# Optimization experiments

Measured on AMD Instinct MI355X. Metric: run time of the kernel, lower is better.

## Reference

```python
import jax, jax.numpy as jnp
import numpy as np

B, T, M = 4, 1024, 512
H, K, V = 8, 64, 64
EPS = 1e-6


def setup_inputs() -> dict:
    key = jax.random.key(0)
    ks = jax.random.split(key, 8)
    s = 1.0 / np.sqrt(M)
    return {
        "query": jax.random.normal(ks[0], (B, T, M), jnp.float32),
        "key": jax.random.normal(ks[1], (B, T, M), jnp.float32),
        "value": jax.random.normal(ks[2], (B, T, M), jnp.float32),
        "Wq": jax.random.normal(ks[3], (M, H * K), jnp.float32) * s,
        "Wk": jax.random.normal(ks[4], (M, H * K), jnp.float32) * s,
        "Wv": jax.random.normal(ks[5], (M, H * V), jnp.float32) * s,
        # gate linear is zero-initialized in the original (Constant(0.0)); use
        # small random weights so the gate path is exercised numerically.
        "Wg": jax.random.normal(ks[6], (M, H * V), jnp.float32) * (0.02 * s),
        "bg": jnp.zeros((H * V,), jnp.float32),
        "Wo": jax.random.normal(ks[7], (H * V, M), jnp.float32) * (1.0 / np.sqrt(H * V)),
    }


def _phi(x):
    return jax.nn.elu(x) + 1.0


def reference(query, key, value, Wq, Wk, Wv, Wg, bg, Wo):
    # projections -> [B, T, H, d]
    q = (query @ Wq).reshape(B, T, H, K)
    k = (key @ Wk).reshape(B, T, H, K)
    v = (value @ Wv).reshape(B, T, H, V)

    qf = _phi(q)
    kf = _phi(k)

    # multiplicative value gate from the raw value input
    gate = jax.nn.sigmoid((value @ Wg + bg).reshape(B, T, H, V))
    v = v * (2.0 * gate)

    # visualization attention map: qf . kf, causal, row-normalized
    scores = jnp.einsum("bthk,bshk->bhts", qf, kf)  # [B,H,T,T]
    causal = (jnp.arange(T)[None, :] <= jnp.arange(T)[:, None]).astype(scores.dtype)
    scores = scores * causal[None, None]
    att_map = scores / (jnp.sum(scores, axis=-1, keepdims=True) + EPS)

    # causal linear attention via cumulative sums (Tq == Tk so the idx-take
    # in the original is an identity gather)
    kv = jnp.einsum("bthk,bthv->bthkv", kf, v)  # [B,T,H,K,V]
    kv_cum = jnp.cumsum(kv, axis=1)
    k_cum = jnp.cumsum(kf, axis=1)               # [B,T,H,K]

    numer = jnp.einsum("bthk,bthkv->bthv", qf, kv_cum)
    denom = jnp.einsum("bthk,bthk->bth", qf, k_cum) + EPS
    out = (numer / denom[..., None]).reshape(B, T, H * V)
    out = out @ Wo  # [B,T,M]
    return out, att_map
```

## Files before the change

### kernel.cpp

```cpp
#include <hip/hip_runtime.h>
#include <cstdint>

#define TDIM 1024
#define BDIM 4
#define EPSF 1e-6f

#define OFF_DEN   0u
#define OFF_KSUM  32768u
#define OFF_KV    65536u
#define FLOAT_BYTES 8650752u
#define UOFF_QP 0u
#define UOFF_KP 2097152u
#define UOFF_VP 4194304u
#define UOFF_NB 6291456u
#define UOFF_WQ 8388608u
#define UOFF_WK 8650752u
#define UOFF_WV 8912896u
#define UOFF_WG 9175040u
#define UOFF_WO 9437184u

typedef short bf16x8 __attribute__((ext_vector_type(8)));
typedef float f32x4  __attribute__((ext_vector_type(4)));
typedef unsigned short ushort_t;

union bfu { int4 i4; unsigned short us[8]; bf16x8 v; };

__device__ __forceinline__ float phi_f(float x)  { return x > 0.f ? x + 1.f : __expf(x); }
__device__ __forceinline__ float sigm_f(float x) { return 1.f / (1.f + __expf(-x)); }
__device__ __forceinline__ unsigned short f2b(float x) {
    union { float f; unsigned u; } v; v.f = x;
    return (unsigned short)((v.u + 0x7FFFu + ((v.u >> 16) & 1u)) >> 16);
}
__device__ __forceinline__ float b2f(unsigned short s) {
    union { unsigned u; float f; } v; v.u = (unsigned)s << 16; return v.f;
}
__device__ __forceinline__ int4 pack8(float4 a, float4 b) {
    bfu u;
    u.us[0] = f2b(a.x); u.us[1] = f2b(a.y); u.us[2] = f2b(a.z); u.us[3] = f2b(a.w);
    u.us[4] = f2b(b.x); u.us[5] = f2b(b.y); u.us[6] = f2b(b.z); u.us[7] = f2b(b.w);
    return u.i4;
}
#define FMA4(ACC, S, V) do { (ACC).x += (S)*(V).x; (ACC).y += (S)*(V).y; \
                             (ACC).z += (S)*(V).z; (ACC).w += (S)*(V).w; } while (0)

__global__ __launch_bounds__(256) void castwt_all(const float* __restrict__ W0,
                                                  const float* __restrict__ W1,
                                                  const float* __restrict__ W2,
                                                  const float* __restrict__ W3,
                                                  const float* __restrict__ W4,
                                                  ushort_t* __restrict__ T0,
                                                  ushort_t* __restrict__ T1,
                                                  ushort_t* __restrict__ T2,
                                                  ushort_t* __restrict__ T3,
                                                  ushort_t* __restrict__ T4) {
    const float* W; ushort_t* Wt;
    switch (blockIdx.z) {
        case 0: W = W0; Wt = T0; break;
        case 1: W = W1; Wt = T1; break;
        case 2: W = W2; Wt = T2; break;
        case 3: W = W3; Wt = T3; break;
        default: W = W4; Wt = T4; break;
    }
    __shared__ unsigned short tile[32][36];
    const int t = threadIdx.x;
    const int r0 = blockIdx.y * 32, c0 = blockIdx.x * 32;
    {
        const int r = t >> 3, c4 = (t & 7) * 4;
        float4 x = *(const float4*)(W + (size_t)(r0 + r) * 512 + c0 + c4);
        tile[c4 + 0][r] = f2b(x.x); tile[c4 + 1][r] = f2b(x.y);
        tile[c4 + 2][r] = f2b(x.z); tile[c4 + 3][r] = f2b(x.w);
    }
    __syncthreads();
    const int c = t >> 3, r4 = (t & 7) * 4;
    ushort4 o;
    o.x = tile[c][r4 + 0]; o.y = tile[c][r4 + 1];
    o.z = tile[c][r4 + 2]; o.w = tile[c][r4 + 3];
    *(ushort4*)(Wt + (size_t)(c0 + c) * 512 + r0 + r4) = o;
}

__global__ __launch_bounds__(256) void proj_k(const float* __restrict__ query,
                                              const float* __restrict__ key_,
                                              const float* __restrict__ value,
                                              const ushort_t* __restrict__ wqt,
                                              const ushort_t* __restrict__ wkt,
                                              const ushort_t* __restrict__ wvt,
                                              const ushort_t* __restrict__ wgt,
                                              const float* __restrict__ bg,
                                              ushort_t* __restrict__ qp,
                                              ushort_t* __restrict__ kp,
                                              ushort_t* __restrict__ vp) {
    __shared__ __align__(16) unsigned short As[2][4096];
    __shared__ __align__(16) unsigned short Bs[2][4096];
    __shared__ __align__(16) unsigned short Bs2[2][4096];
    const int z = blockIdx.z;
    const float* A = (z == 0) ? query : (z == 1) ? key_ : value;
    const ushort_t* B0 = (z == 0) ? wqt : (z == 1) ? wkt : wvt;
    ushort_t* outp = (z == 0) ? qp : (z == 1) ? kp : vp;
    const bool dual = (z == 2);

    const int tid = threadIdx.x;
    const int row0 = blockIdx.x * 64, n0 = blockIdx.y * 64;
    const int w = tid >> 6, lane = tid & 63;
    const int cc = tid & 7, rr = tid >> 3;
    const int fm = lane & 15, fq = lane >> 4;
    const int la0 = (cc * 64 + (rr ^ cc)) * 8;
    const int la1 = (cc * 64 + ((rr + 32) ^ cc)) * 8;

    f32x4 acc[4], acc2[4];
#pragma unroll
    for (int i = 0; i < 4; i++) {
        acc[i]  = (f32x4){0.f, 0.f, 0.f, 0.f};
        acc2[i] = (f32x4){0.f, 0.f, 0.f, 0.f};
    }

    const float*   aptr = A  + (size_t)(row0 + rr) * 512 + cc * 8;
    const ushort_t* bptr = B0 + (size_t)(n0 + rr) * 512 + cc * 8;
    const ushort_t* gptr = wgt + (size_t)(n0 + rr) * 512 + cc * 8;

    float4 a0 = *(const float4*)(aptr);
    float4 a1 = *(const float4*)(aptr + 4);
    float4 a2 = *(const float4*)(aptr + 32 * 512);
    float4 a3 = *(const float4*)(aptr + 32 * 512 + 4);
    int4 b0 = *(const int4*)(bptr);
    int4 b1 = *(const int4*)(bptr + 32 * 512);
    int4 g0 = {0, 0, 0, 0}, g1 = {0, 0, 0, 0};
    if (dual) { g0 = *(const int4*)(gptr); g1 = *(const int4*)(gptr + 32 * 512); }
    *(int4*)&As[0][la0] = pack8(a0, a1);
    *(int4*)&As[0][la1] = pack8(a2, a3);
    *(int4*)&Bs[0][la0] = b0; *(int4*)&Bs[0][la1] = b1;
    if (dual) { *(int4*)&Bs2[0][la0] = g0; *(int4*)&Bs2[0][la1] = g1; }
    __syncthreads();

    for (int kti = 0; kti < 8; kti++) {
        const int buf = kti & 1;
        if (kti < 7) {
            const int off = (kti + 1) * 64;
            a0 = *(const float4*)(aptr + off);
            a1 = *(const float4*)(aptr + off + 4);
            a2 = *(const float4*)(aptr + off + 32 * 512);
            a3 = *(const float4*)(aptr + off + 32 * 512 + 4);
            b0 = *(const int4*)(bptr + off);
            b1 = *(const int4*)(bptr + off + 32 * 512);
            if (dual) {
                g0 = *(const int4*)(gptr + off);
                g1 = *(const int4*)(gptr + off + 32 * 512);
            }
        }
        if (dual) {
#pragma unroll
            for (int j = 0; j < 2; j++) {
                const int cu = j * 4 + fq;
                bf16x8 af = *(const bf16x8*)&As[buf][(cu * 64 + ((w * 16 + fm) ^ cu)) * 8];
#pragma unroll
                for (int nb = 0; nb < 4; nb++) {
                    bf16x8 bv = *(const bf16x8*)&Bs[buf][(cu * 64 + ((nb * 16 + fm) ^ cu)) * 8];
                    bf16x8 gv = *(const bf16x8*)&Bs2[buf][(cu * 64 + ((nb * 16 + fm) ^ cu)) * 8];
                    acc[nb]  = __builtin_amdgcn_mfma_f32_16x16x32_bf16(af, bv, acc[nb], 0, 0, 0);
                    acc2[nb] = __builtin_amdgcn_mfma_f32_16x16x32_bf16(af, gv, acc2[nb], 0, 0, 0);
                }
            }
        } else {
#pragma unroll
            for (int j = 0; j < 2; j++) {
                const int cu = j * 4 + fq;
                bf16x8 af = *(const bf16x8*)&As[buf][(cu * 64 + ((w * 16 + fm) ^ cu)) * 8];
#pragma unroll
                for (int nb = 0; nb < 4; nb++) {
                    bf16x8 bv = *(const bf16x8*)&Bs[buf][(cu * 64 + ((nb * 16 + fm) ^ cu)) * 8];
                    acc[nb] = __builtin_amdgcn_mfma_f32_16x16x32_bf16(af, bv, acc[nb], 0, 0, 0);
                }
            }
        }
        if (kti < 7) {
            const int nb_ = buf ^ 1;
            *(int4*)&As[nb_][la0] = pack8(a0, a1);
            *(int4*)&As[nb_][la1] = pack8(a2, a3);
            *(int4*)&Bs[nb_][la0] = b0; *(int4*)&Bs[nb_][la1] = b1;
            if (dual) { *(int4*)&Bs2[nb_][la0] = g0; *(int4*)&Bs2[nb_][la1] = g1; }
            __syncthreads();
        }
    }

#pragma unroll
    for (int nb = 0; nb < 4; nb++) {
        const int col = n0 + nb * 16 + fm;
        const float bb = dual ? bg[col] : 0.f;
#pragma unroll
        for (int r = 0; r < 4; r++) {
            const int row = row0 + w * 16 + fq * 4 + r;
            const float v = acc[nb][r];
            const ushort_t o = dual ? f2b(v * 2.f * sigm_f(acc2[nb][r] + bb))
                                    : f2b(phi_f(v));
            outp[(size_t)row * 512 + col] = o;
        }
    }
}

__global__ __launch_bounds__(256) void outproj_k(const ushort_t* __restrict__ A,
                                                 const ushort_t* __restrict__ Bt,
                                                 float* __restrict__ out) {
    __shared__ __align__(16) unsigned short As[2][4096];
    __shared__ __align__(16) unsigned short Bs[2][4096];
    const int tid = threadIdx.x;
    const int row0 = blockIdx.x * 64, n0 = blockIdx.y * 64;
    const int w = tid >> 6, lane = tid & 63;
    const int cc = tid & 7, rr = tid >> 3;
    const int fm = lane & 15, fq = lane >> 4;
    const int la0 = (cc * 64 + (rr ^ cc)) * 8;
    const int la1 = (cc * 64 + ((rr + 32) ^ cc)) * 8;

    f32x4 acc[4];
#pragma unroll
    for (int i = 0; i < 4; i++) acc[i] = (f32x4){0.f, 0.f, 0.f, 0.f};

    const ushort_t* aptr = A  + (size_t)(row0 + rr) * 512 + cc * 8;
    const ushort_t* bptr = Bt + (size_t)(n0 + rr) * 512 + cc * 8;
    int4 ra0 = *(const int4*)(aptr);
    int4 ra1 = *(const int4*)(aptr + 32 * 512);
    int4 rb0 = *(const int4*)(bptr);
    int4 rb1 = *(const int4*)(bptr + 32 * 512);
    *(int4*)&As[0][la0] = ra0; *(int4*)&As[0][la1] = ra1;
    *(int4*)&Bs[0][la0] = rb0; *(int4*)&Bs[0][la1] = rb1;
    __syncthreads();

    for (int kti = 0; kti < 8; kti++) {
        const int buf = kti & 1;
        if (kti < 7) {
            const int off = (kti + 1) * 64;
            ra0 = *(const int4*)(aptr + off);
            ra1 = *(const int4*)(aptr + off + 32 * 512);
            rb0 = *(const int4*)(bptr + off);
            rb1 = *(const int4*)(bptr + off + 32 * 512);
        }
#pragma unroll
        for (int j = 0; j < 2; j++) {
            const int cu = j * 4 + fq;
            bf16x8 af = *(const bf16x8*)&As[buf][(cu * 64 + ((w * 16 + fm) ^ cu)) * 8];
#pragma unroll
            for (int nb = 0; nb < 4; nb++) {
                bf16x8 bv = *(const bf16x8*)&Bs[buf][(cu * 64 + ((nb * 16 + fm) ^ cu)) * 8];
                acc[nb] = __builtin_amdgcn_mfma_f32_16x16x32_bf16(af, bv, acc[nb], 0, 0, 0);
            }
        }
        if (kti < 7) {
            const int nb_ = buf ^ 1;
            *(int4*)&As[nb_][la0] = ra0; *(int4*)&As[nb_][la1] = ra1;
            *(int4*)&Bs[nb_][la0] = rb0; *(int4*)&Bs[nb_][la1] = rb1;
            __syncthreads();
        }
    }
#pragma unroll
    for (int nb = 0; nb < 4; nb++) {
        const int col = n0 + nb * 16 + fm;
#pragma unroll
        for (int r = 0; r < 4; r++) {
            const int row = row0 + w * 16 + fq * 4 + r;
            __builtin_nontemporal_store(acc[nb][r], &out[(size_t)row * 512 + col]);
        }
    }
}

__global__ __launch_bounds__(256) void chunksum_k(const ushort_t* __restrict__ kb,
                                                  const ushort_t* __restrict__ vb,
                                                  float* __restrict__ kv,
                                                  float* __restrict__ ksum) {
    __shared__ __align__(16) float kf_c[64][68];
    __shared__ __align__(16) float vg_c[64][68];
    const int tid = threadIdx.x;
    const int bh = blockIdx.x, c = blockIdx.y;
    const int b = bh >> 3, h = bh & 7;
    const int r = tid >> 2, qq = tid & 3;
    {
        const size_t rowbase = ((size_t)(b * TDIM + c * 64 + r)) * 512 + h * 64 + qq * 16;
        bfu k0, k1, v0, v1;
        k0.i4 = *(const int4*)(kb + rowbase);
        k1.i4 = *(const int4*)(kb + rowbase + 8);
        v0.i4 = *(const int4*)(vb + rowbase);
        v1.i4 = *(const int4*)(vb + rowbase + 8);
#pragma unroll
        for (int j = 0; j < 8; j++) {
            kf_c[r][qq * 16 + j]     = b2f(k0.us[j]);
            kf_c[r][qq * 16 + 8 + j] = b2f(k1.us[j]);
            vg_c[r][qq * 16 + j]     = b2f(v0.us[j]);
            vg_c[r][qq * 16 + 8 + j] = b2f(v1.us[j]);
        }
    }
    __syncthreads();
    const int k0i = (tid >> 4) * 4;
    const int v0i = (tid & 15) * 4;
    float4 a4[4];
#pragma unroll
    for (int i = 0; i < 4; i++) a4[i] = make_float4(0.f, 0.f, 0.f, 0.f);
    for (int t = 0; t < 64; t++) {
        float4 kk4 = *(const float4*)&kf_c[t][k0i];
        float4 vv  = *(const float4*)&vg_c[t][v0i];
        FMA4(a4[0], kk4.x, vv); FMA4(a4[1], kk4.y, vv);
        FMA4(a4[2], kk4.z, vv); FMA4(a4[3], kk4.w, vv);
    }
    const size_t base = (size_t)(bh * 16 + c) * 64;
#pragma unroll
    for (int i = 0; i < 4; i++)
        *(float4*)(kv + (base + k0i + i) * 64 + v0i) = a4[i];
    if (tid < 64) {
        float s = 0.f;
        for (int t = 0; t < 64; t++) s += kf_c[t][tid];
        ksum[base + tid] = s;
    }
}

__global__ __launch_bounds__(256) void prefix_k(float* __restrict__ kv,
                                                float* __restrict__ ksum) {
    const int tid = threadIdx.x;
    const int bh = blockIdx.x;
    float4 run[4];
#pragma unroll
    for (int u = 0; u < 4; u++) run[u] = make_float4(0.f, 0.f, 0.f, 0.f);
    const int d0 = tid * 16;
    for (int c = 0; c < 16; c++) {
        float* p = kv + (size_t)(bh * 16 + c) * 4096 + d0;
#pragma unroll
        for (int u = 0; u < 4; u++) {
            float4 x = *(float4*)(p + 4 * u);
            *(float4*)(p + 4 * u) = run[u];
            run[u].x += x.x; run[u].y += x.y; run[u].z += x.z; run[u].w += x.w;
        }
    }
    if (tid < 64) {
        float r2 = 0.f;
        for (int c = 0; c < 16; c++) {
            float* p = ksum + (size_t)(bh * 16 + c) * 64 + tid;
            float x = *p; *p = r2; r2 += x;
        }
    }
}

__global__ __launch_bounds__(256) void chunkout_k(const ushort_t* __restrict__ qb,
                                                  const ushort_t* __restrict__ kb,
                                                  const ushort_t* __restrict__ vb,
                                                  const float* __restrict__ kvp,
                                                  const float* __restrict__ ksum,
                                                  ushort_t* __restrict__ nbo,
                                                  float* __restrict__ denom) {
    __shared__ __align__(16) unsigned short qs[4096];
    __shared__ __align__(16) unsigned short ks[4096];
    __shared__ __align__(16) unsigned short vs[4096];
    __shared__ __align__(16) unsigned short kvs[4096];
    __shared__ __align__(16) float sc[64][68];
    __shared__ __align__(16) float kpre[64];
    __shared__ __align__(16) float ps[64][4];
    __shared__ __align__(16) float inv_s[64];
    const int tid = threadIdx.x;
    const int bh = blockIdx.x, c = blockIdx.y;
    const int b = bh >> 3, h = bh & 7;
    const int w = tid >> 6, lane = tid & 63;
    const int fm = lane & 15, fq = lane >> 4;

    {
        const int rr = tid >> 3, cc = tid & 7;
        const ushort_t* qp = qb + ((size_t)(b * TDIM + c * 64 + rr)) * 512 + h * 64 + cc * 8;
        const ushort_t* kp = kb + ((size_t)(b * TDIM + c * 64 + rr)) * 512 + h * 64 + cc * 8;
        *(int4*)&qs[(cc * 64 + (rr ^ cc)) * 8]        = *(const int4*)qp;
        *(int4*)&qs[(cc * 64 + ((rr + 32) ^ cc)) * 8] = *(const int4*)(qp + 32 * 512);
        *(int4*)&ks[(cc * 64 + (rr ^ cc)) * 8]        = *(const int4*)kp;
        *(int4*)&ks[(cc * 64 + ((rr + 32) ^ cc)) * 8] = *(const int4*)(kp + 32 * 512);
        const int v = tid & 63, su0 = (tid >> 6) * 2;
#pragma unroll
        for (int e = 0; e < 2; e++) {
            const int su = su0 + e;
            bfu t1;
#pragma unroll
            for (int j = 0; j < 8; j++)
                t1.us[j] = vb[((size_t)(b * TDIM + c * 64 + su * 8 + j)) * 512 + h * 64 + v];
            *(int4*)&vs[(su * 64 + (v ^ su)) * 8] = t1.i4;
            bfu t2;
            const float* kvrow = kvp + (size_t)(bh * 16 + c) * 4096 + v;
#pragma unroll
            for (int j = 0; j < 8; j++)
                t2.us[j] = f2b(kvrow[(su * 8 + j) * 64]);
            *(int4*)&kvs[(su * 64 + (v ^ su)) * 8] = t2.i4;
        }
        if (tid < 64) kpre[tid] = ksum[(size_t)(bh * 16 + c) * 64 + tid];
    }
    __syncthreads();

    {
        f32x4 sa[4];
#pragma unroll
        for (int i = 0; i < 4; i++) sa[i] = (f32x4){0.f, 0.f, 0.f, 0.f};
#pragma unroll
        for (int j = 0; j < 2; j++) {
            const int cu = j * 4 + fq;
            bf16x8 aq = *(const bf16x8*)&qs[(cu * 64 + ((w * 16 + fm) ^ cu)) * 8];
#pragma unroll
            for (int nb = 0; nb < 4; nb++) {
                bf16x8 bk = *(const bf16x8*)&ks[(cu * 64 + ((nb * 16 + fm) ^ cu)) * 8];
                sa[nb] = __builtin_amdgcn_mfma_f32_16x16x32_bf16(aq, bk, sa[nb], 0, 0, 0);
            }
        }
#pragma unroll
        for (int nb = 0; nb < 4; nb++) {
            const int s_l = nb * 16 + fm;
#pragma unroll
            for (int r = 0; r < 4; r++) {
                const int t_l = w * 16 + fq * 4 + r;
                sc[t_l][s_l] = (s_l <= t_l) ? sa[nb][r] : 0.f;
            }
        }
    }
    __syncthreads();

    {
        const int rw = tid >> 2, sq = tid & 3;
        float p = 0.f;
#pragma unroll
        for (int s = sq * 16; s < sq * 16 + 16; s++) p += sc[rw][s];
#pragma unroll
        for (int kd = sq * 16; kd < sq * 16 + 16; kd++) {
            const int cu = kd >> 3;
            p += b2f(qs[(cu * 64 + (rw ^ cu)) * 8 + (kd & 7)]) * kpre[kd];
        }
        ps[rw][sq] = p;
    }
    __syncthreads();
    {
        const int rw = tid >> 2, sq = tid & 3;
        if (sq == 0) {
            float den = ps[rw][0] + ps[rw][1] + ps[rw][2] + ps[rw][3];
            denom[(size_t)bh * TDIM + c * 64 + rw] = den;
            inv_s[rw] = 1.f / (den + EPSF);
        }
    }
    __syncthreads();

    {
        f32x4 oa[4];
#pragma unroll
        for (int i = 0; i < 4; i++) oa[i] = (f32x4){0.f, 0.f, 0.f, 0.f};
        bf16x8 aq[2], ap_[2];
#pragma unroll
        for (int j = 0; j < 2; j++) {
            const int cu = j * 4 + fq;
            aq[j] = *(const bf16x8*)&qs[(cu * 64 + ((w * 16 + fm) ^ cu)) * 8];
            bfu t;
#pragma unroll
            for (int e2 = 0; e2 < 8; e2++) t.us[e2] = f2b(sc[w * 16 + fm][cu * 8 + e2]);
            ap_[j] = t.v;
        }
#pragma unroll
        for (int nb = 0; nb < 4; nb++) {
#pragma unroll
            for (int j = 0; j < 2; j++) {
                const int cu = j * 4 + fq;
                bf16x8 bkv = *(const bf16x8*)&kvs[(cu * 64 + ((nb * 16 + fm) ^ cu)) * 8];
                bf16x8 bv  = *(const bf16x8*)&vs[(cu * 64 + ((nb * 16 + fm) ^ cu)) * 8];
                oa[nb] = __builtin_amdgcn_mfma_f32_16x16x32_bf16(aq[j], bkv, oa[nb], 0, 0, 0);
                oa[nb] = __builtin_amdgcn_mfma_f32_16x16x32_bf16(ap_[j], bv, oa[nb], 0, 0, 0);
            }
        }
#pragma unroll
        for (int nb = 0; nb < 4; nb++) {
            const int vcol = nb * 16 + fm;
#pragma unroll
            for (int r = 0; r < 4; r++) {
                const int t_l = w * 16 + fq * 4 + r;
                const float val = oa[nb][r] * inv_s[t_l];
                nbo[((size_t)(b * TDIM + c * 64 + t_l)) * 512 + h * 64 + vcol] = f2b(val);
            }
        }
    }
}

__global__ __launch_bounds__(256) void attmap_k(const ushort_t* __restrict__ qb,
                                                const ushort_t* __restrict__ kb,
                                                const float* __restrict__ denom,
                                                float* __restrict__ att) {
    __shared__ __align__(16) unsigned short qs[4096];
    __shared__ __align__(16) unsigned short ks[2][4096];
    __shared__ __align__(16) float inv_s[64];
    const int tid = threadIdx.x;
    const int bh = blockIdx.x, diag = blockIdx.y;
    const int tt0 = diag * 64;
    const int b = bh >> 3, h = bh & 7;
    const int w = tid >> 6, lane = tid & 63;
    const int fm = lane & 15, fq = lane >> 4;
    const int rr = tid >> 3, cc = tid & 7;
    const int la0 = (cc * 64 + (rr ^ cc)) * 8;
    const int la1 = (cc * 64 + ((rr + 32) ^ cc)) * 8;

    const ushort_t* qptr = qb + ((size_t)(b * TDIM + tt0 + rr)) * 512 + h * 64 + cc * 8;
    const ushort_t* kbase = kb + ((size_t)(b * TDIM + rr)) * 512 + h * 64 + cc * 8;
    *(int4*)&qs[la0] = *(const int4*)qptr;
    *(int4*)&qs[la1] = *(const int4*)(qptr + 32 * 512);
    int4 rk0 = *(const int4*)(kbase);
    int4 rk1 = *(const int4*)(kbase + 32 * 512);
    *(int4*)&ks[0][la0] = rk0;
    *(int4*)&ks[0][la1] = rk1;
    if (tid < 64) inv_s[tid] = 1.f / (denom[(size_t)bh * TDIM + tt0 + tid] + EPSF);
    __syncthreads();

    bf16x8 aq[2];
    float invr[4];
#pragma unroll
    for (int j = 0; j < 2; j++) {
        const int cu = j * 4 + fq;
        aq[j] = *(const bf16x8*)&qs[(cu * 64 + ((w * 16 + fm) ^ cu)) * 8];
    }
#pragma unroll
    for (int r = 0; r < 4; r++) invr[r] = inv_s[w * 16 + fq * 4 + r];

    float* attb = att + (size_t)bh * TDIM * TDIM;
    for (int st = 0; st <= diag; st++) {
        const int buf = st & 1;
        if (st < diag) {
            const size_t off = (size_t)(st + 1) * 64 * 512;
            rk0 = *(const int4*)(kbase + off);
            rk1 = *(const int4*)(kbase + off + 32 * 512);
        }
        f32x4 sa[4];
#pragma unroll
        for (int i = 0; i < 4; i++) sa[i] = (f32x4){0.f, 0.f, 0.f, 0.f};
#pragma unroll
        for (int j = 0; j < 2; j++) {
            const int cu = j * 4 + fq;
#pragma unroll
            for (int nb = 0; nb < 4; nb++) {
                bf16x8 bk = *(const bf16x8*)&ks[buf][(cu * 64 + ((nb * 16 + fm) ^ cu)) * 8];
                sa[nb] = __builtin_amdgcn_mfma_f32_16x16x32_bf16(aq[j], bk, sa[nb], 0, 0, 0);
            }
        }
        const int s0 = st * 64;
        if (st < diag) {
#pragma unroll
            for (int nb = 0; nb < 4; nb++) {
                const int s_g = s0 + nb * 16 + fm;
#pragma unroll
                for (int r = 0; r < 4; r++) {
                    const int t_g = tt0 + w * 16 + fq * 4 + r;
                    __builtin_nontemporal_store(sa[nb][r] * invr[r],
                                                &attb[(size_t)t_g * TDIM + s_g]);
                }
            }
            *(int4*)&ks[buf ^ 1][la0] = rk0;
            *(int4*)&ks[buf ^ 1][la1] = rk1;
            __syncthreads();
        } else {
#pragma unroll
            for (int nb = 0; nb < 4; nb++) {
                const int s_l = nb * 16 + fm;
#pragma unroll
                for (int r = 0; r < 4; r++) {
                    const int t_l = w * 16 + fq * 4 + r;
                    const float val = (s_l <= t_l) ? sa[nb][r] * invr[r] : 0.f;
                    __builtin_nontemporal_store(val,
                        &attb[(size_t)(tt0 + t_l) * TDIM + s0 + s_l]);
                }
            }
        }
    }
    {
        const f32x4 z = (f32x4){0.f, 0.f, 0.f, 0.f};
        const int r = tid >> 2, qq = tid & 3;
        float* rowp = attb + (size_t)(tt0 + r) * TDIM;
        for (int c0 = (diag + 1) * 64 + qq * 4; c0 < TDIM; c0 += 16)
            __builtin_nontemporal_store(z, (f32x4*)(rowp + c0));
    }
}

extern "C" void kernel_launch(void* const* d_in, const int* in_sizes, int n_in,
                              void* d_out, int out_size, void* d_ws, size_t ws_size,
                              hipStream_t stream) {
    (void)in_sizes; (void)n_in; (void)out_size; (void)ws_size;
    const float* query = (const float*)d_in[0];
    const float* key   = (const float*)d_in[1];
    const float* value = (const float*)d_in[2];
    const float* Wq    = (const float*)d_in[3];
    const float* Wk    = (const float*)d_in[4];
    const float* Wv    = (const float*)d_in[5];
    const float* Wg    = (const float*)d_in[6];
    const float* bg    = (const float*)d_in[7];
    const float* Wo    = (const float*)d_in[8];
    float* out = (float*)d_out;
    float* att = (float*)d_out + 2097152;
    float* ws  = (float*)d_ws;
    float* den  = ws + OFF_DEN;
    float* ksum = ws + OFF_KSUM;
    float* kv   = ws + OFF_KV;
    ushort_t* ub  = (ushort_t*)((char*)d_ws + FLOAT_BYTES);
    ushort_t* qp  = ub + UOFF_QP;
    ushort_t* kp  = ub + UOFF_KP;
    ushort_t* vp  = ub + UOFF_VP;
    ushort_t* nbp = ub + UOFF_NB;
    ushort_t* wqt = ub + UOFF_WQ;
    ushort_t* wkt = ub + UOFF_WK;
    ushort_t* wvt = ub + UOFF_WV;
    ushort_t* wgt = ub + UOFF_WG;
    ushort_t* wot = ub + UOFF_WO;

    dim3 blk(256);
    castwt_all<<<dim3(16, 16, 5), blk, 0, stream>>>(Wq, Wk, Wv, Wg, Wo,
                                                    wqt, wkt, wvt, wgt, wot);
    proj_k<<<dim3(64, 8, 3), blk, 0, stream>>>(query, key, value,
                                               wqt, wkt, wvt, wgt, bg, qp, kp, vp);
    chunksum_k<<<dim3(32, 16), blk, 0, stream>>>(kp, vp, kv, ksum);
    prefix_k<<<dim3(32), blk, 0, stream>>>(kv, ksum);
    chunkout_k<<<dim3(32, 16), blk, 0, stream>>>(qp, kp, vp, kv, ksum, nbp, den);
    attmap_k<<<dim3(32, 16), blk, 0, stream>>>(qp, kp, den, att);
    outproj_k<<<dim3(64, 8), blk, 0, stream>>>(nbp, wot, out);
}
```

Before: 266.1 us.

## Fuse prefix scan, chunk output and attention-map kernels into one kernel

Replaces the prefix_k, chunkout_k and attmap_k kernels with a single fused_k kernel. Each block recomputes its exclusive prefix of chunk KV states and k-sums by summing the earlier chunks directly, which removes the serial prefix kernel. It also reuses the diagonal score tile for the denominator, the output and the attention-map row, and schedules the heaviest diagonals first. In exchange it does redundant prefix summation of up to 15 chunk states per block and uses about 70 KB of dynamic shared memory, which may limit occupancy.

Measured after the change: 245.0 us. 7.9% less time.

```diff
diff --git a/kernel.cpp b/kernel.cpp
--- a/kernel.cpp
+++ b/kernel.cpp
@@ -5,7 +5,6 @@
 #define BDIM 4
 #define EPSF 1e-6f
 
-#define OFF_DEN   0u
 #define OFF_KSUM  32768u
 #define OFF_KV    65536u
 #define FLOAT_BYTES 8650752u
@@ -308,177 +307,25 @@
     }
 }
 
-__global__ __launch_bounds__(256) void prefix_k(float* __restrict__ kv,
-                                                float* __restrict__ ksum) {
+__global__ __launch_bounds__(256) void fused_k(const ushort_t* __restrict__ qb,
+                                               const ushort_t* __restrict__ kb,
+                                               const ushort_t* __restrict__ vb,
+                                               const float* __restrict__ kvc,
+                                               const float* __restrict__ ksum,
+                                               ushort_t* __restrict__ nbo,
+                                               float* __restrict__ att) {
+    extern __shared__ __align__(16) char smem[];
+    unsigned short* qs   = (unsigned short*)smem;
+    unsigned short* ksb  = qs + 4096;
+    unsigned short* vrow = ksb + 8192;
+    float* kvf  = (float*)(vrow + 64 * 72);
+    float* sc   = kvf + 64 * 68;
+    float* kpre = sc + 64 * 68;
+    float* ps   = kpre + 64;
+    float* inv_s = ps + 256;
+
     const int tid = threadIdx.x;
-    const int bh = blockIdx.x;
-    float4 run[4];
-#pragma unroll
-    for (int u = 0; u < 4; u++) run[u] = make_float4(0.f, 0.f, 0.f, 0.f);
-    const int d0 = tid * 16;
-    for (int c = 0; c < 16; c++) {
-        float* p = kv + (size_t)(bh * 16 + c) * 4096 + d0;
-#pragma unroll
-        for (int u = 0; u < 4; u++) {
-            float4 x = *(float4*)(p + 4 * u);
-            *(float4*)(p + 4 * u) = run[u];
-            run[u].x += x.x; run[u].y += x.y; run[u].z += x.z; run[u].w += x.w;
-        }
-    }
-    if (tid < 64) {
-        float r2 = 0.f;
-        for (int c = 0; c < 16; c++) {
-            float* p = ksum + (size_t)(bh * 16 + c) * 64 + tid;
-            float x = *p; *p = r2; r2 += x;
-        }
-    }
-}
-
-__global__ __launch_bounds__(256) void chunkout_k(const ushort_t* __restrict__ qb,
-                                                  const ushort_t* __restrict__ kb,
-                                                  const ushort_t* __restrict__ vb,
-                                                  const float* __restrict__ kvp,
-                                                  const float* __restrict__ ksum,
-                                                  ushort_t* __restrict__ nbo,
-                                                  float* __restrict__ denom) {
-    __shared__ __align__(16) unsigned short qs[4096];
-    __shared__ __align__(16) unsigned short ks[4096];
-    __shared__ __align__(16) unsigned short vs[4096];
-    __shared__ __align__(16) unsigned short kvs[4096];
-    __shared__ __align__(16) float sc[64][68];
-    __shared__ __align__(16) float kpre[64];
-    __shared__ __align__(16) float ps[64][4];
-    __shared__ __align__(16) float inv_s[64];
-    const int tid = threadIdx.x;
-    const int bh = blockIdx.x, c = blockIdx.y;
-    const int b = bh >> 3, h = bh & 7;
-    const int w = tid >> 6, lane = tid & 63;
-    const int fm = lane & 15, fq = lane >> 4;
-
-    {
-        const int rr = tid >> 3, cc = tid & 7;
-        const ushort_t* qp = qb + ((size_t)(b * TDIM + c * 64 + rr)) * 512 + h * 64 + cc * 8;
-        const ushort_t* kp = kb + ((size_t)(b * TDIM + c * 64 + rr)) * 512 + h * 64 + cc * 8;
-        *(int4*)&qs[(cc * 64 + (rr ^ cc)) * 8]        = *(const int4*)qp;
-        *(int4*)&qs[(cc * 64 + ((rr + 32) ^ cc)) * 8] = *(const int4*)(qp + 32 * 512);
-        *(int4*)&ks[(cc * 64 + (rr ^ cc)) * 8]        = *(const int4*)kp;
-        *(int4*)&ks[(cc * 64 + ((rr + 32) ^ cc)) * 8] = *(const int4*)(kp + 32 * 512);
-        const int v = tid & 63, su0 = (tid >> 6) * 2;
-#pragma unroll
-        for (int e = 0; e < 2; e++) {
-            const int su = su0 + e;
-            bfu t1;
-#pragma unroll
-            for (int j = 0; j < 8; j++)
-                t1.us[j] = vb[((size_t)(b * TDIM + c * 64 + su * 8 + j)) * 512 + h * 64 + v];
-            *(int4*)&vs[(su * 64 + (v ^ su)) * 8] = t1.i4;
-            bfu t2;
-            const float* kvrow = kvp + (size_t)(bh * 16 + c) * 4096 + v;
-#pragma unroll
-            for (int j = 0; j < 8; j++)
-                t2.us[j] = f2b(kvrow[(su * 8 + j) * 64]);
-            *(int4*)&kvs[(su * 64 + (v ^ su)) * 8] = t2.i4;
-        }
-        if (tid < 64) kpre[tid] = ksum[(size_t)(bh * 16 + c) * 64 + tid];
-    }
-    __syncthreads();
-
-    {
-        f32x4 sa[4];
-#pragma unroll
-        for (int i = 0; i < 4; i++) sa[i] = (f32x4){0.f, 0.f, 0.f, 0.f};
-#pragma unroll
-        for (int j = 0; j < 2; j++) {
-            const int cu = j * 4 + fq;
-            bf16x8 aq = *(const bf16x8*)&qs[(cu * 64 + ((w * 16 + fm) ^ cu)) * 8];
-#pragma unroll
-            for (int nb = 0; nb < 4; nb++) {
-                bf16x8 bk = *(const bf16x8*)&ks[(cu * 64 + ((nb * 16 + fm) ^ cu)) * 8];
-                sa[nb] = __builtin_amdgcn_mfma_f32_16x16x32_bf16(aq, bk, sa[nb], 0, 0, 0);
-            }
-        }
-#pragma unroll
-        for (int nb = 0; nb < 4; nb++) {
-            const int s_l = nb * 16 + fm;
-#pragma unroll
-            for (int r = 0; r < 4; r++) {
-                const int t_l = w * 16 + fq * 4 + r;
-                sc[t_l][s_l] = (s_l <= t_l) ? sa[nb][r] : 0.f;
-            }
-        }
-    }
-    __syncthreads();
-
-    {
-        const int rw = tid >> 2, sq = tid & 3;
-        float p = 0.f;
-#pragma unroll
-        for (int s = sq * 16; s < sq * 16 + 16; s++) p += sc[rw][s];
-#pragma unroll
-        for (int kd = sq * 16; kd < sq * 16 + 16; kd++) {
-            const int cu = kd >> 3;
-            p += b2f(qs[(cu * 64 + (rw ^ cu)) * 8 + (kd & 7)]) * kpre[kd];
-        }
-        ps[rw][sq] = p;
-    }
-    __syncthreads();
-    {
-        const int rw = tid >> 2, sq = tid & 3;
-        if (sq == 0) {
-            float den = ps[rw][0] + ps[rw][1] + ps[rw][2] + ps[rw][3];
-            denom[(size_t)bh * TDIM + c * 64 + rw] = den;
-            inv_s[rw] = 1.f / (den + EPSF);
-        }
-    }
-    __syncthreads();
-
-    {
-        f32x4 oa[4];
-#pragma unroll
-        for (int i = 0; i < 4; i++) oa[i] = (f32x4){0.f, 0.f, 0.f, 0.f};
-        bf16x8 aq[2], ap_[2];
-#pragma unroll
-        for (int j = 0; j < 2; j++) {
-            const int cu = j * 4 + fq;
-            aq[j] = *(const bf16x8*)&qs[(cu * 64 + ((w * 16 + fm) ^ cu)) * 8];
-            bfu t;
-#pragma unroll
-            for (int e2 = 0; e2 < 8; e2++) t.us[e2] = f2b(sc[w * 16 + fm][cu * 8 + e2]);
-            ap_[j] = t.v;
-        }
-#pragma unroll
-        for (int nb = 0; nb < 4; nb++) {
-#pragma unroll
-            for (int j = 0; j < 2; j++) {
-                const int cu = j * 4 + fq;
-                bf16x8 bkv = *(const bf16x8*)&kvs[(cu * 64 + ((nb * 16 + fm) ^ cu)) * 8];
-                bf16x8 bv  = *(const bf16x8*)&vs[(cu * 64 + ((nb * 16 + fm) ^ cu)) * 8];
-                oa[nb] = __builtin_amdgcn_mfma_f32_16x16x32_bf16(aq[j], bkv, oa[nb], 0, 0, 0);
-                oa[nb] = __builtin_amdgcn_mfma_f32_16x16x32_bf16(ap_[j], bv, oa[nb], 0, 0, 0);
-            }
-        }
-#pragma unroll
-        for (int nb = 0; nb < 4; nb++) {
-            const int vcol = nb * 16 + fm;
-#pragma unroll
-            for (int r = 0; r < 4; r++) {
-                const int t_l = w * 16 + fq * 4 + r;
-                const float val = oa[nb][r] * inv_s[t_l];
-                nbo[((size_t)(b * TDIM + c * 64 + t_l)) * 512 + h * 64 + vcol] = f2b(val);
-            }
-        }
-    }
-}
-
-__global__ __launch_bounds__(256) void attmap_k(const ushort_t* __restrict__ qb,
-                                                const ushort_t* __restrict__ kb,
-                                                const float* __restrict__ denom,
-                                                float* __restrict__ att) {
-    __shared__ __align__(16) unsigned short qs[4096];
-    __shared__ __align__(16) unsigned short ks[2][4096];
-    __shared__ __align__(16) float inv_s[64];
-    const int tid = threadIdx.x;
-    const int bh = blockIdx.x, diag = blockIdx.y;
+    const int bh = blockIdx.x, diag = 15 - (int)blockIdx.y;
     const int tt0 = diag * 64;
     const int b = bh >> 3, h = bh & 7;
     const int w = tid >> 6, lane = tid & 63;
@@ -487,16 +334,139 @@
     const int la0 = (cc * 64 + (rr ^ cc)) * 8;
     const int la1 = (cc * 64 + ((rr + 32) ^ cc)) * 8;
 
-    const ushort_t* qptr = qb + ((size_t)(b * TDIM + tt0 + rr)) * 512 + h * 64 + cc * 8;
     const ushort_t* kbase = kb + ((size_t)(b * TDIM + rr)) * 512 + h * 64 + cc * 8;
-    *(int4*)&qs[la0] = *(const int4*)qptr;
-    *(int4*)&qs[la1] = *(const int4*)(qptr + 32 * 512);
-    int4 rk0 = *(const int4*)(kbase);
-    int4 rk1 = *(const int4*)(kbase + 32 * 512);
-    *(int4*)&ks[0][la0] = rk0;
-    *(int4*)&ks[0][la1] = rk1;
-    if (tid < 64) inv_s[tid] = 1.f / (denom[(size_t)bh * TDIM + tt0 + tid] + EPSF);
-    __syncthreads();
+
+    {
+        const ushort_t* qptr = qb + ((size_t)(b * TDIM + tt0 + rr)) * 512 + h * 64 + cc * 8;
+        *(int4*)&qs[la0] = *(const int4*)qptr;
+        *(int4*)&qs[la1] = *(const int4*)(qptr + 32 * 512);
+        const ushort_t* kptr = kbase + (size_t)tt0 * 512;
+        *(int4*)&ksb[la0] = *(const int4*)kptr;
+        *(int4*)&ksb[la1] = *(const int4*)(kptr + 32 * 512);
+        const int r = tid >> 2, qq = tid & 3;
+        const ushort_t* vptr = vb + ((size_t)(b * TDIM + tt0 + r)) * 512 + h * 64 + qq * 16;
+        *(int4*)&vrow[r * 72 + qq * 16]     = *(const int4*)vptr;
+        *(int4*)&vrow[r * 72 + qq * 16 + 8] = *(const int4*)(vptr + 8);
+        float4 a4[4];
+#pragma unroll
+        for (int u = 0; u < 4; u++) a4[u] = make_float4(0.f, 0.f, 0.f, 0.f);
+        for (int c2 = 0; c2 < diag; c2++) {
+            const float* p = kvc + (size_t)(bh * 16 + c2) * 4096 + r * 64 + qq * 16;
+#pragma unroll
+            for (int u = 0; u < 4; u++) {
+                float4 x = *(const float4*)(p + 4 * u);
+                a4[u].x += x.x; a4[u].y += x.y; a4[u].z += x.z; a4[u].w += x.w;
+            }
+        }
+#pragma unroll
+        for (int u = 0; u < 4; u++) *(float4*)&kvf[r * 68 + qq * 16 + 4 * u] = a4[u];
+        if (tid < 64) {
+            float s = 0.f;
+            for (int c2 = 0; c2 < diag; c2++)
+                s += ksum[(size_t)(bh * 16 + c2) * 64 + tid];
+            kpre[tid] = s;
+        }
+    }
+    __syncthreads();
+
+    f32x4 sa[4];
+    {
+        int4 rk0 = {0,0,0,0}, rk1 = {0,0,0,0};
+        if (diag > 0) {
+            rk0 = *(const int4*)(kbase);
+            rk1 = *(const int4*)(kbase + 32 * 512);
+        }
+#pragma unroll
+        for (int i = 0; i < 4; i++) sa[i] = (f32x4){0.f, 0.f, 0.f, 0.f};
+#pragma unroll
+        for (int j = 0; j < 2; j++) {
+            const int cu = j * 4 + fq;
+            bf16x8 aqf = *(const bf16x8*)&qs[(cu * 64 + ((w * 16 + fm) ^ cu)) * 8];
+#pragma unroll
+            for (int nb = 0; nb < 4; nb++) {
+                bf16x8 bk = *(const bf16x8*)&ksb[(cu * 64 + ((nb * 16 + fm) ^ cu)) * 8];
+                sa[nb] = __builtin_amdgcn_mfma_f32_16x16x32_bf16(aqf, bk, sa[nb], 0, 0, 0);
+            }
+        }
+#pragma unroll
+        for (int nb = 0; nb < 4; nb++) {
+            const int s_l = nb * 16 + fm;
+#pragma unroll
+            for (int r = 0; r < 4; r++) {
+                const int t_l = w * 16 + fq * 4 + r;
+                sc[t_l * 68 + s_l] = (s_l <= t_l) ? sa[nb][r] : 0.f;
+            }
+        }
+        if (diag > 0) {
+            *(int4*)&ksb[4096 + la0] = rk0;
+            *(int4*)&ksb[4096 + la1] = rk1;
+        }
+    }
+    __syncthreads();
+
+    {
+        const int rw = tid >> 2, sq = tid & 3;
+        float p = 0.f;
+#pragma unroll
+        for (int s = sq * 16; s < sq * 16 + 16; s++) p += sc[rw * 68 + s];
+#pragma unroll
+        for (int kd = sq * 16; kd < sq * 16 + 16; kd++) {
+            const int cu = kd >> 3;
+            p += b2f(qs[(cu * 64 + (rw ^ cu)) * 8 + (kd & 7)]) * kpre[kd];
+        }
+        ps[rw * 4 + sq] = p;
+    }
+    __syncthreads();
+    {
+        const int rw = tid >> 2, sq = tid & 3;
+        if (sq == 0) {
+            float den = ps[rw * 4] + ps[rw * 4 + 1] + ps[rw * 4 + 2] + ps[rw * 4 + 3];
+            inv_s[rw] = 1.f / (den + EPSF);
+        }
+    }
+    __syncthreads();
+
+    {
+        f32x4 oa[4];
+#pragma unroll
+        for (int i = 0; i < 4; i++) oa[i] = (f32x4){0.f, 0.f, 0.f, 0.f};
+        bf16x8 aqv[2], apv[2];
+#pragma unroll
+        for (int j = 0; j < 2; j++) {
+            const int cu = j * 4 + fq;
+            aqv[j] = *(const bf16x8*)&qs[(cu * 64 + ((w * 16 + fm) ^ cu)) * 8];
+            bfu t;
+#pragma unroll
+            for (int e2 = 0; e2 < 8; e2++) t.us[e2] = f2b(sc[(w * 16 + fm) * 68 + cu * 8 + e2]);
+            apv[j] = t.v;
+        }
+#pragma unroll
+        for (int nb = 0; nb < 4; nb++) {
+            const int v = nb * 16 + fm;
+#pragma unroll
+            for (int j = 0; j < 2; j++) {
+                const int cu = j * 4 + fq;
+                bfu tkv, tv;
+#pragma unroll
+                for (int e = 0; e < 8; e++) {
+                    tkv.us[e] = f2b(kvf[(cu * 8 + e) * 68 + v]);
+                    tv.us[e]  = vrow[(cu * 8 + e) * 72 + v];
+                }
+                oa[nb] = __builtin_amdgcn_mfma_f32_16x16x32_bf16(aqv[j], tkv.v, oa[nb], 0, 0, 0);
+                oa[nb] = __builtin_amdgcn_mfma_f32_16x16x32_bf16(apv[j], tv.v, oa[nb], 0, 0, 0);
+            }
+        }
+#pragma unroll
+        for (int nb = 0; nb < 4; nb++) {
+            const int vcol = nb * 16 + fm;
+#pragma unroll
+            for (int r = 0; r < 4; r++) {
+                const int t_l = w * 16 + fq * 4 + r;
+                const float val = oa[nb][r] * inv_s[t_l];
+                nbo[((size_t)(b * TDIM + tt0 + t_l)) * 512 + h * 64 + vcol] = f2b(val);
+            }
+        }
+    }
 
     bf16x8 aq[2];
     float invr[4];
@@ -509,52 +479,53 @@
     for (int r = 0; r < 4; r++) invr[r] = inv_s[w * 16 + fq * 4 + r];
 
     float* attb = att + (size_t)bh * TDIM * TDIM;
-    for (int st = 0; st <= diag; st++) {
-        const int buf = st & 1;
-        if (st < diag) {
+    int4 rk0, rk1;
+    for (int st = 0; st < diag; st++) {
+        const int bsel = (st + 1) & 1;
+        if (st + 1 < diag) {
             const size_t off = (size_t)(st + 1) * 64 * 512;
             rk0 = *(const int4*)(kbase + off);
             rk1 = *(const int4*)(kbase + off + 32 * 512);
         }
-        f32x4 sa[4];
-#pragma unroll
-        for (int i = 0; i < 4; i++) sa[i] = (f32x4){0.f, 0.f, 0.f, 0.f};
+        f32x4 pa[4];
+#pragma unroll
+        for (int i = 0; i < 4; i++) pa[i] = (f32x4){0.f, 0.f, 0.f, 0.f};
 #pragma unroll
         for (int j = 0; j < 2; j++) {
             const int cu = j * 4 + fq;
 #pragma unroll
             for (int nb = 0; nb < 4; nb++) {
-                bf16x8 bk = *(const bf16x8*)&ks[buf][(cu * 64 + ((nb * 16 + fm) ^ cu)) * 8];
-                sa[nb] = __builtin_amdgcn_mfma_f32_16x16x32_bf16(aq[j], bk, sa[nb], 0, 0, 0);
+                bf16x8 bk = *(const bf16x8*)&ksb[bsel * 4096 +
+                                                 (cu * 64 + ((nb * 16 + fm) ^ cu)) * 8];
+                pa[nb] = __builtin_amdgcn_mfma_f32_16x16x32_bf16(aq[j], bk, pa[nb], 0, 0, 0);
             }
         }
         const int s0 = st * 64;
-        if (st < diag) {
-#pragma unroll
-            for (int nb = 0; nb < 4; nb++) {
-                const int s_g = s0 + nb * 16 + fm;
-#pragma unroll
-                for (int r = 0; r < 4; r++) {
-                    const int t_g = tt0 + w * 16 + fq * 4 + r;
-                    __builtin_nontemporal_store(sa[nb][r] * invr[r],
-                                                &attb[(size_t)t_g * TDIM + s_g]);
-                }
-            }
-            *(int4*)&ks[buf ^ 1][la0] = rk0;
-            *(int4*)&ks[buf ^ 1][la1] = rk1;
+#pragma unroll
+        for (int nb = 0; nb < 4; nb++) {
+            const int s_g = s0 + nb * 16 + fm;
+#pragma unroll
+            for (int r = 0; r < 4; r++) {
+                const int t_g = tt0 + w * 16 + fq * 4 + r;
+                __builtin_nontemporal_store(pa[nb][r] * invr[r],
+                                            &attb[(size_t)t_g * TDIM + s_g]);
+            }
+        }
+        if (st + 1 < diag) {
+            *(int4*)&ksb[(bsel ^ 1) * 4096 + la0] = rk0;
+            *(int4*)&ksb[(bsel ^ 1) * 4096 + la1] = rk1;
             __syncthreads();
-        } else {
-#pragma unroll
-            for (int nb = 0; nb < 4; nb++) {
-                const int s_l = nb * 16 + fm;
-#pragma unroll
-                for (int r = 0; r < 4; r++) {
-                    const int t_l = w * 16 + fq * 4 + r;
-                    const float val = (s_l <= t_l) ? sa[nb][r] * invr[r] : 0.f;
-                    __builtin_nontemporal_store(val,
-                        &attb[(size_t)(tt0 + t_l) * TDIM + s0 + s_l]);
-                }
-            }
+        }
+    }
+#pragma unroll
+    for (int nb = 0; nb < 4; nb++) {
+        const int s_l = nb * 16 + fm;
+#pragma unroll
+        for (int r = 0; r < 4; r++) {
+            const int t_l = w * 16 + fq * 4 + r;
+            const float val = (s_l <= t_l) ? sa[nb][r] * invr[r] : 0.f;
+            __builtin_nontemporal_store(val,
+                &attb[(size_t)(tt0 + t_l) * TDIM + tt0 + s_l]);
         }
     }
     {
@@ -582,7 +553,6 @@
     float* out = (float*)d_out;
     float* att = (float*)d_out + 2097152;
     float* ws  = (float*)d_ws;
-    float* den  = ws + OFF_DEN;
     float* ksum = ws + OFF_KSUM;
     float* kv   = ws + OFF_KV;
     ushort_t* ub  = (ushort_t*)((char*)d_ws + FLOAT_BYTES);
@@ -602,8 +572,6 @@
     proj_k<<<dim3(64, 8, 3), blk, 0, stream>>>(query, key, value,
                                                wqt, wkt, wvt, wgt, bg, qp, kp, vp);
     chunksum_k<<<dim3(32, 16), blk, 0, stream>>>(kp, vp, kv, ksum);
-    prefix_k<<<dim3(32), blk, 0, stream>>>(kv, ksum);
-    chunkout_k<<<dim3(32, 16), blk, 0, stream>>>(qp, kp, vp, kv, ksum, nbp, den);
-    attmap_k<<<dim3(32, 16), blk, 0, stream>>>(qp, kp, den, att);
+    fused_k<<<dim3(32, 16), blk, 70144, stream>>>(qp, kp, vp, kv, ksum, nbp, att);
     outproj_k<<<dim3(64, 8), blk, 0, stream>>>(nbp, wot, out);
 }
```
